# Optimization experiments

Hardware: AMD Instinct MI355X
Metric: run time of the kernel (lower is better)

The kernel has to match this reference:

```python
import jax, jax.numpy as jnp
import numpy as np

B, C, H, W = 4, 3, 1024, 1024


def softsplat_sum(im, flow):
    """Summation forward-warp (softsplat, no metric): bilinear scatter-add.
    im: [B,C,H,W], flow: [B,2,H,W] (flow[:,0]=dx, flow[:,1]=dy)."""
    b, c, h, w = im.shape
    n = h * w
    X = jnp.arange(w, dtype=flow.dtype)[None, None, :] + flow[:, 0]  # [B,H,W]
    Y = jnp.arange(h, dtype=flow.dtype)[None, :, None] + flow[:, 1]  # [B,H,W]
    x0 = jnp.floor(X); y0 = jnp.floor(Y)
    x1 = x0 + 1.0;     y1 = y0 + 1.0
    # bilinear weights for the 4 surrounding integer pixels: NW, NE, SW, SE
    ws = jnp.stack([(x1 - X) * (y1 - Y), (X - x0) * (y1 - Y),
                    (x1 - X) * (Y - y0), (X - x0) * (Y - y0)])  # [4,B,H,W]
    xi = jnp.stack([x0, x1, x0, x1]).astype(jnp.int32)
    yi = jnp.stack([y0, y0, y1, y1]).astype(jnp.int32)
    valid = (xi >= 0) & (xi < w) & (yi >= 0) & (yi < h)
    ws = jnp.where(valid, ws, 0.0)
    idx = jnp.clip(yi, 0, h - 1) * w + jnp.clip(xi, 0, w - 1)     # [4,B,H,W]
    idx = idx.reshape(4, b, n).transpose(1, 0, 2)                  # [B,4,N]
    ws = ws.reshape(4, b, n).transpose(1, 0, 2)                    # [B,4,N]
    imf = im.reshape(b, c, n)

    def splat_one(imf_b, idx_b, w_b):
        vals = (imf_b[:, None, :] * w_b[None]).reshape(c, 4 * n)   # [C,4N]
        return jnp.zeros((c, n), imf_b.dtype).at[:, idx_b.reshape(-1)].add(vals)

    out = jax.vmap(splat_one)(imf, idx, ws)                        # [B,C,N]
    return out.reshape(b, c, h, w)


def setup_inputs() -> dict:
    key = jax.random.key(0)
    k1, k2, k3, k4 = jax.random.split(key, 4)
    flows = 5.0 * jax.random.normal(k1, (2, B, 2, H, W), jnp.float32)
    im0 = jax.random.uniform(k2, (B, C, H, W), jnp.float32)
    im1 = jax.random.uniform(k3, (B, C, H, W), jnp.float32)
    t_value = 0.2 + 0.6 * jax.random.uniform(k4, (B,), jnp.float32)
    return {"flows": flows, "im0": im0, "im1": im1, "t_value": t_value}


def reference(flows, im0, im1, t_value):
    t = t_value.reshape(-1, 1, 1, 1)
    warped_fir = softsplat_sum(im0, (1.0 / t) * flows[0])
    warped_sec = softsplat_sum(im1, (1.0 / (1.0 - t)) * flows[1])
    loss = jnp.mean(jnp.abs(warped_fir - im1)) + jnp.mean(jnp.abs(warped_sec - im0))
    return loss
```

## Files before the change

### kernel.cpp

```cpp
#include <hip/hip_runtime.h>

#define BN 4
#define CN 3
#define HN 1024
#define WN 1024
#define HW (HN * WN)
#define BHW (BN * HW)
#define TOT (BN * CN * HW)

#define TS 64
#define TXN 16
#define TYN 16
#define NTB 256
#define NTILE 1024
#define CHUNK 4096
#define NCHB 1024
#define NPAIR 8

#define OFF_GCNT 0
#define OFF_LOSS 8192
#define OFF_TICK 8200
#define OFF_BORD 8448
#define SZ_BORDR (BN * 16 * 1024 * 8)
#define OFF_REC  (OFF_BORD + 4 * SZ_BORDR)

#define INV_BSCALE (1.0f / 65536.0f)
#define FMASK 0x1FFFFFull

#define PQ 252.0f
#define INV_PQ (1.0f / 252.0f)
#define VQ 4095.0f
#define VSCL (65536.0f / 4095.0f)

__device__ __forceinline__ float blockReduce4(float local, float* smem) {
#pragma unroll
    for (int off = 32; off > 0; off >>= 1)
        local += __shfl_down(local, off, 64);
    int wave = threadIdx.x >> 6;
    if ((threadIdx.x & 63) == 0) smem[wave] = local;
    __syncthreads();
    float s = 0.0f;
    if (threadIdx.x == 0)
        s = smem[0] + smem[1] + smem[2] + smem[3];
    return s;
}

__global__ __launch_bounds__(256) void p1_kernel(
    const float* __restrict__ flows,
    const float* __restrict__ im0,
    const float* __restrict__ im1,
    const float* __restrict__ tv,
    unsigned int* __restrict__ gcnt,
    unsigned long long* __restrict__ rec,
    int cap, int dirsel)
{
    __shared__ unsigned int cnt[NTB];
    __shared__ unsigned int off[NTB];
    __shared__ unsigned int sexc[NTB];
    __shared__ unsigned int stot;
    __shared__ unsigned char sbkt[CHUNK];
    __shared__ unsigned long long stage[CHUNK];
    int tid = threadIdx.x;
    cnt[tid] = 0;
    __syncthreads();

    int bid = blockIdx.x;
    int dir, chunk;
    if (dirsel == 2) { dir = bid >> 10; chunk = bid & 1023; }
    else             { dir = dirsel;    chunk = bid; }

    const float* flow = flows + (size_t)dir * (BN * 2 * HW);
    const float* im   = dir ? im1 : im0;
    unsigned int* gk  = gcnt + dir * NTILE;
    unsigned long long* recd =
        rec + (size_t)((dirsel == 2) ? dir : 0) * NTILE * (size_t)cap;

    int base = chunk * CHUNK;
    int b = base >> 20;
    int pb = base - b * HW;
    float t = tv[b];
    float s = dir ? (1.0f / (1.0f - t)) : (1.0f / t);
    const float2* fxp = (const float2*)(flow + (size_t)(b * 2 + 0) * HW);
    const float2* fyp = (const float2*)(flow + (size_t)(b * 2 + 1) * HW);
    const float2* v0p = (const float2*)(im + (size_t)(b * 3 + 0) * HW);
    const float2* v1p = (const float2*)(im + (size_t)(b * 3 + 1) * HW);
    const float2* v2p = (const float2*)(im + (size_t)(b * 3 + 2) * HW);

    unsigned sc[2 * NPAIR];
    unsigned long long pay[2 * NPAIR];

#pragma unroll
    for (int i = 0; i < NPAIR; ++i) {
        int p0 = pb + 2 * tid + i * 512;
        int y = p0 >> 10;
        int x = p0 & 1023;
        int e = p0 >> 1;
        float2 fx2 = fxp[e], fy2 = fyp[e];
        float2 c02 = v0p[e], c12 = v1p[e], c22 = v2p[e];
        float Xh[2], Yh[2], vv0[2], vv1[2], vv2[2];
        Xh[0] = (float)x + s * fx2.x;        Xh[1] = (float)(x + 1) + s * fx2.y;
        Yh[0] = (float)y + s * fy2.x;        Yh[1] = (float)y + s * fy2.y;
        vv0[0] = c02.x; vv0[1] = c02.y;
        vv1[0] = c12.x; vv1[1] = c12.y;
        vv2[0] = c22.x; vv2[1] = c22.y;
        int kk[2]; bool val[2];
#pragma unroll
        for (int h = 0; h < 2; ++h) {
            int x0 = (int)floorf(Xh[h]);
            int y0 = (int)floorf(Yh[h]);
            val[h] = !(x0 < -1 || x0 > WN - 1 || y0 < -1 || y0 > HN - 1);
            int bx = (x0 < 0 ? 0 : x0) >> 6;
            int by = (y0 < 0 ? 0 : y0) >> 6;
            kk[h] = (by << 4) + bx;
            float lx = Xh[h] - (float)(bx << 6);
            float ly = Yh[h] - (float)(by << 6);
            unsigned long long lq = __float2uint_rn((lx + 1.0f) * PQ);
            unsigned long long mq = __float2uint_rn((ly + 1.0f) * PQ);
            unsigned long long q0 = __float2uint_rn(vv0[h] * VQ);
            unsigned long long q1 = __float2uint_rn(vv1[h] * VQ);
            unsigned long long q2 = __float2uint_rn(vv2[h] * VQ);
            pay[2 * i + h] = lq | (mq << 14) | (q0 << 28) | (q1 << 40) | (q2 << 52);
        }
        if (val[0] & val[1] & (kk[0] == kk[1])) {
            unsigned ls = atomicAdd(&cnt[kk[0]], 2u);
            sc[2 * i]     = ((unsigned)kk[0] << 16) | ls;
            sc[2 * i + 1] = ((unsigned)kk[0] << 16) | (ls + 1u);
        } else {
            sc[2 * i]     = val[0] ? (((unsigned)kk[0] << 16) | atomicAdd(&cnt[kk[0]], 1u))
                                   : 0xFFFFFFFFu;
            sc[2 * i + 1] = val[1] ? (((unsigned)kk[1] << 16) | atomicAdd(&cnt[kk[1]], 1u))
                                   : 0xFFFFFFFFu;
        }
    }
    __syncthreads();

    unsigned c = cnt[tid];
    unsigned g = c ? atomicAdd(&gk[b * NTB + tid], c) : 0u;
    if (tid < 64) {
        unsigned v0 = cnt[4 * tid], v1 = cnt[4 * tid + 1];
        unsigned v2 = cnt[4 * tid + 2], v3 = cnt[4 * tid + 3];
        unsigned s01 = v0 + v1;
        unsigned tot = s01 + v2 + v3;
        unsigned run = tot;
#pragma unroll
        for (int d = 1; d < 64; d <<= 1) {
            unsigned u = __shfl_up(run, d, 64);
            if (tid >= d) run += u;
        }
        unsigned excl = run - tot;
        sexc[4 * tid]     = excl;
        sexc[4 * tid + 1] = excl + v0;
        sexc[4 * tid + 2] = excl + s01;
        sexc[4 * tid + 3] = excl + s01 + v2;
        if (tid == 63) stot = run;
    }
    off[tid] = g;
    __syncthreads();

#pragma unroll
    for (int j = 0; j < 2 * NPAIR; ++j) {
        unsigned scv = sc[j];
        if (scv == 0xFFFFFFFFu) continue;
        unsigned k = scv >> 16;
        unsigned pos = sexc[k] + (scv & 0xFFFFu);
        stage[pos] = pay[j];
        sbkt[pos] = (unsigned char)k;
    }
    __syncthreads();

    unsigned T = stot;
    for (unsigned j = tid; j < T; j += 256) {
        int k2 = sbkt[j];
        unsigned slot = off[k2] + (j - sexc[k2]);
        if (slot < (unsigned)cap)
            recd[(size_t)(b * NTB + k2) * (size_t)cap + slot] = stage[j];
    }
}

__global__ __launch_bounds__(256) void p2_kernel(
    const unsigned long long* __restrict__ rec,
    const unsigned int* __restrict__ gcnt,
    const float* __restrict__ im0,
    const float* __restrict__ im1,
    unsigned long long* __restrict__ bord,
    double* __restrict__ loss,
    int cap, int dirsel)
{
    __shared__ unsigned long long tileu[65 * 65];
    __shared__ float smem4[4];
    int kb = blockIdx.x;
    int dir, k;
    if (dirsel == 2) { dir = kb >> 10; k = kb & 1023; }
    else             { dir = dirsel;   k = kb; }
    const float* ref = dir ? im0 : im1;
    const unsigned long long* recd =
        rec + (size_t)((dirsel == 2) ? dir : 0) * NTILE * (size_t)cap;
    unsigned long long* rowacc = bord + (size_t)(2 * dir)     * (BN * 16 * 1024);
    unsigned long long* colacc = bord + (size_t)(2 * dir + 1) * (BN * 16 * 1024);

    int b  = k >> 8;
    int by = (k >> 4) & 15;
    int bx = k & 15;
    int tx = bx << 6, ty = by << 6;
    int tid = threadIdx.x;

    for (int i = tid; i < 65 * 65; i += 256) tileu[i] = 0ull;
    __syncthreads();

    unsigned n = gcnt[dir * NTILE + k];
    if (n > (unsigned)cap) n = cap;
    const unsigned long long* rk = recd + (size_t)k * (size_t)cap;
    for (unsigned r = tid; r < n; r += 256) {
        unsigned long long w = rk[r];
        float lx = (float)(unsigned)(w & 0x3FFFu)         * INV_PQ - 1.0f;
        float ly = (float)(unsigned)((w >> 14) & 0x3FFFu) * INV_PQ - 1.0f;
        float v0s = (float)(unsigned)((w >> 28) & 0xFFFu) * VSCL;
        float v1s = (float)(unsigned)((w >> 40) & 0xFFFu) * VSCL;
        float v2s = (float)(unsigned)((w >> 52) & 0xFFFu) * VSCL;
        int i0 = (int)floorf(lx); if (i0 > 63) i0 = 63;
        int j0 = (int)floorf(ly); if (j0 > 63) j0 = 63;
        float fx = lx - (float)i0;
        float fy = ly - (float)j0;
        float wx0 = 1.0f - fx, wy0 = 1.0f - fy;
#pragma unroll
        for (int c = 0; c < 4; ++c) {
            int ii = i0 + (c & 1), jj = j0 + (c >> 1);
            float w4 = (c & 1 ? fx : wx0) * (c >> 1 ? fy : wy0);
            if (ii >= 0 && jj >= 0 && tx + ii < WN && ty + jj < HN) {
                unsigned long long pk =
                      (unsigned long long)__float2uint_rn(v0s * w4)
                    | ((unsigned long long)__float2uint_rn(v1s * w4) << 21)
                    | ((unsigned long long)__float2uint_rn(v2s * w4) << 42);
                atomicAdd(&tileu[jj * 65 + ii], pk);
            }
        }
    }
    __syncthreads();

    float local = 0.0f;
    for (int c = tid; c < 65 * 65; c += 256) {
        int j = c / 65, i = c - j * 65;
        int gx = tx + i, gy = ty + j;
        if (gx >= WN || gy >= HN) continue;
        unsigned long long a = tileu[c];
        bool fin_i = (i >= 1 || bx == 0) && (i <= 63);
        bool fin_j = (j >= 1 || by == 0) && (j <= 63);
        if (fin_i && fin_j) {
            float a0 = (float)(unsigned)(a & FMASK)         * INV_BSCALE;
            float a1 = (float)(unsigned)((a >> 21) & FMASK) * INV_BSCALE;
            float a2 = (float)(unsigned)((a >> 42) & FMASK) * INV_BSCALE;
            size_t o = (size_t)gy * WN + gx;
            local += fabsf(a0 - ref[(size_t)(b * 3 + 0) * HW + o])
                   + fabsf(a1 - ref[(size_t)(b * 3 + 1) * HW + o])
                   + fabsf(a2 - ref[(size_t)(b * 3 + 2) * HW + o]);
        } else if (a) {
            if ((gy & 63) == 0 && gy >= 64)
                atomicAdd(&rowacc[((size_t)(b * 16 + (gy >> 6)) << 10) + gx], a);
            else
                atomicAdd(&colacc[((size_t)(b * 16 + (gx >> 6)) << 10) + gy], a);
        }
    }
    float ssum = blockReduce4(local, smem4);
    if (tid == 0) unsafeAtomicAdd(loss, (double)ssum);
}

__global__ __launch_bounds__(256) void border_kernel(
    const unsigned long long* __restrict__ bord,
    const float* __restrict__ ref0,
    const float* __restrict__ ref1,
    double* __restrict__ loss,
    unsigned int* __restrict__ ticket,
    float* __restrict__ out)
{
    __shared__ float smem4[4];
    int idx = blockIdx.x * 256 + threadIdx.x;
    int reg = idx >> 16;
    int e = idx & 0xFFFF;
    bool isrow = (reg & 1) == 0;
    const float* ref = (reg < 2) ? ref0 : ref1;
    unsigned long long a = bord[idx];
    int b = e >> 14;
    int rc = (e >> 10) & 15;
    int q = e & 1023;
    float local = 0.0f;
    bool process;
    int gx, gy;
    if (isrow) { process = (rc >= 1); gy = rc << 6; gx = q; }
    else       { process = (rc >= 1) && !(((q & 63) == 0) && q >= 64); gx = rc << 6; gy = q; }
    if (process && a) {
        float a0 = (float)(unsigned)(a & FMASK)         * INV_BSCALE;
        float a1 = (float)(unsigned)((a >> 21) & FMASK) * INV_BSCALE;
        float a2 = (float)(unsigned)((a >> 42) & FMASK) * INV_BSCALE;
        size_t o = (size_t)gy * WN + gx;
        local += fabsf(a0 - ref[(size_t)(b * 3 + 0) * HW + o])
               + fabsf(a1 - ref[(size_t)(b * 3 + 1) * HW + o])
               + fabsf(a2 - ref[(size_t)(b * 3 + 2) * HW + o]);
    } else if (process) {
        size_t o = (size_t)gy * WN + gx;
        local += fabsf(ref[(size_t)(b * 3 + 0) * HW + o])
               + fabsf(ref[(size_t)(b * 3 + 1) * HW + o])
               + fabsf(ref[(size_t)(b * 3 + 2) * HW + o]);
    }
    float ssum = blockReduce4(local, smem4);
    if (threadIdx.x == 0) {
        unsafeAtomicAdd(loss, (double)ssum);
        __threadfence();
        unsigned tkt = atomicAdd(ticket, 1u);
        if (tkt == gridDim.x - 1) {
            double v = unsafeAtomicAdd(loss, 0.0);
            out[0] = (float)(v / (double)TOT);
        }
    }
}

#define FPSCALE 65536.0f
#define INV_FPSCALE (1.0f / 65536.0f)

__device__ __forceinline__ unsigned long long pack3f(float c0, float c1, float c2, float w) {
    unsigned long long f0 = (unsigned long long)__float2uint_rn(c0 * w * FPSCALE);
    unsigned long long f1 = (unsigned long long)__float2uint_rn(c1 * w * FPSCALE);
    unsigned long long f2 = (unsigned long long)__float2uint_rn(c2 * w * FPSCALE);
    return f0 | (f1 << 21) | (f2 << 42);
}

__global__ __launch_bounds__(256) void splat_kernel(
    const float* __restrict__ flow, const float* __restrict__ im,
    const float* __restrict__ tv, unsigned long long* __restrict__ acc, int invert)
{
    int gid = blockIdx.x * blockDim.x + threadIdx.x;
    if (gid >= BHW) return;
    int b = gid / HW;
    int p = gid - b * HW;
    int y = p >> 10, x = p & 1023;
    float t = tv[b];
    float s = invert ? (1.0f / (1.0f - t)) : (1.0f / t);
    float X = (float)x + s * flow[(size_t)(b * 2 + 0) * HW + p];
    float Y = (float)y + s * flow[(size_t)(b * 2 + 1) * HW + p];
    float x0f = floorf(X), y0f = floorf(Y);
    int x0 = (int)x0f, y0 = (int)y0f;
    float fx = X - x0f, fy = Y - y0f;
    float wx0 = 1.0f - fx, wx1 = fx, wy0 = 1.0f - fy, wy1 = fy;
    float v0 = im[(size_t)(b * 3 + 0) * HW + p];
    float v1 = im[(size_t)(b * 3 + 1) * HW + p];
    float v2 = im[(size_t)(b * 3 + 2) * HW + p];
    bool vx0 = (x0 >= 0) & (x0 < WN);
    bool vx1 = (x0 + 1 >= 0) & (x0 + 1 < WN);
    unsigned long long* accb = acc + (size_t)b * HW;
#pragma unroll
    for (int r = 0; r < 2; ++r) {
        int yi = y0 + r;
        if (yi < 0 || yi >= HN) continue;
        float wy = r ? wy1 : wy0;
        size_t rowbase = (size_t)yi * WN;
        if (vx0) atomicAdd(&accb[rowbase + x0],     pack3f(v0, v1, v2, wx0 * wy));
        if (vx1) atomicAdd(&accb[rowbase + x0 + 1], pack3f(v0, v1, v2, wx1 * wy));
    }
}

__global__ __launch_bounds__(256) void loss_kernel(
    unsigned long long* __restrict__ acc, const float* __restrict__ ref,
    double* __restrict__ loss)
{
    __shared__ float smem4[4];
    int stride = gridDim.x * blockDim.x;
    float local = 0.0f;
    for (int i = blockIdx.x * blockDim.x + threadIdx.x; i < BHW; i += stride) {
        int b = i / HW;
        int p = i - b * HW;
        unsigned long long a = acc[i];
        acc[i] = 0ull;
        float c0 = (float)(unsigned)(a & FMASK)         * INV_FPSCALE;
        float c1 = (float)(unsigned)((a >> 21) & FMASK) * INV_FPSCALE;
        float c2 = (float)(unsigned)((a >> 42) & FMASK) * INV_FPSCALE;
        local += fabsf(c0 - ref[(size_t)(b * 3 + 0) * HW + p])
               + fabsf(c1 - ref[(size_t)(b * 3 + 1) * HW + p])
               + fabsf(c2 - ref[(size_t)(b * 3 + 2) * HW + p]);
    }
    float ssum = blockReduce4(local, smem4);
    if (threadIdx.x == 0) unsafeAtomicAdd(loss, (double)ssum);
}

__global__ void finalize_kernel(const double* __restrict__ loss,
                                float* __restrict__ out)
{
    out[0] = (float)(loss[0] / (double)TOT);
}

extern "C" void kernel_launch(void* const* d_in, const int* in_sizes, int n_in,
                              void* d_out, int out_size, void* d_ws, size_t ws_size,
                              hipStream_t stream)
{
    const float* flows = (const float*)d_in[0];
    const float* im0   = (const float*)d_in[1];
    const float* im1   = (const float*)d_in[2];
    const float* tv    = (const float*)d_in[3];
    const float* flows1 = flows + (size_t)BN * 2 * HW;
    const int threads = 256;

    long long avail = (long long)ws_size - (long long)OFF_REC;
    int capBoth = 0, capSeq = 0;
    if (avail > 0) {
        long long cb = avail / (2LL * NTILE * 8);
        long long cs = avail / ((long long)NTILE * 8);
        capBoth = (int)(cb > 8192 ? 8192 : cb);
        capSeq  = (int)(cs > 8192 ? 8192 : cs);
    }

    char* ws = (char*)d_ws;
    unsigned int* gcnt = (unsigned int*)(ws + OFF_GCNT);
    double* loss = (double*)(ws + OFF_LOSS);
    unsigned int* ticket = (unsigned int*)(ws + OFF_TICK);
    unsigned long long* bord = (unsigned long long*)(ws + OFF_BORD);
    unsigned long long* rec = (unsigned long long*)(ws + OFF_REC);

    if (capBoth >= 5120) {
        hipMemsetAsync(d_ws, 0, OFF_REC, stream);
        p1_kernel<<<2 * NCHB, threads, 0, stream>>>(flows, im0, im1, tv,
                                                    gcnt, rec, capBoth, 2);
        p2_kernel<<<2 * NTILE, threads, 0, stream>>>(rec, gcnt, im0, im1,
                                                     bord, loss, capBoth, 2);
        border_kernel<<<1024, threads, 0, stream>>>(bord, im1, im0, loss,
                                                    ticket, (float*)d_out);
    } else if (capSeq >= 5120) {
        hipMemsetAsync(d_ws, 0, OFF_REC, stream);
        p1_kernel<<<NCHB, threads, 0, stream>>>(flows, im0, im1, tv,
                                                gcnt, rec, capSeq, 0);
        p2_kernel<<<NTILE, threads, 0, stream>>>(rec, gcnt, im0, im1,
                                                 bord, loss, capSeq, 0);
        p1_kernel<<<NCHB, threads, 0, stream>>>(flows, im0, im1, tv,
                                                gcnt, rec, capSeq, 1);
        p2_kernel<<<NTILE, threads, 0, stream>>>(rec, gcnt, im0, im1,
                                                 bord, loss, capSeq, 1);
        border_kernel<<<1024, threads, 0, stream>>>(bord, im1, im0, loss,
                                                    ticket, (float*)d_out);
    } else {
        unsigned long long* acc = (unsigned long long*)d_ws;
        double* lss = (double*)(acc + (size_t)BN * HW);
        hipMemsetAsync(d_ws, 0, sizeof(unsigned long long) * (size_t)BN * HW + sizeof(double), stream);
        const int sgrid = (BHW + threads - 1) / threads;
        splat_kernel<<<sgrid, threads, 0, stream>>>(flows, im0, tv, acc, 0);
        loss_kernel<<<2048, threads, 0, stream>>>(acc, im1, lss);
        splat_kernel<<<sgrid, threads, 0, stream>>>(flows1, im1, tv, acc, 1);
        loss_kernel<<<2048, threads, 0, stream>>>(acc, im0, lss);
        finalize_kernel<<<1, 1, 0, stream>>>(lss, (float*)d_out);
    }
}
```

Measured before the change: 296.9 us.

## Fuse bin, tile-splat and border passes into one persistent kernel with grid barriers

```diff
diff --git a/kernel.cpp b/kernel.cpp
--- a/kernel.cpp
+++ b/kernel.cpp
@@ -16,10 +16,13 @@
 #define CHUNK 4096
 #define NCHB 1024
 #define NPAIR 8
+#define NBLK 1024
 
 #define OFF_GCNT 0
 #define OFF_LOSS 8192
 #define OFF_TICK 8200
+#define OFF_BAR1 8204
+#define OFF_BAR2 8208
 #define OFF_BORD 8448
 #define SZ_BORDR (BN * 16 * 1024 * 8)
 #define OFF_REC  (OFF_BORD + 4 * SZ_BORDR)
@@ -32,6 +35,22 @@
 #define VQ 4095.0f
 #define VSCL (65536.0f / 4095.0f)
 
+struct P1Sh {
+    unsigned int cnt[NTB];
+    unsigned int off[NTB];
+    unsigned int sexc[NTB];
+    unsigned int stot;
+    unsigned char sbkt[CHUNK];
+    unsigned long long stage[CHUNK];
+};
+struct Sh {
+    union {
+        P1Sh p1;
+        unsigned long long tileu[65 * 65];
+    } u;
+    float smem4[4];
+};
+
 __device__ __forceinline__ float blockReduce4(float local, float* smem) {
 #pragma unroll
     for (int off = 32; off > 0; off >>= 1)
@@ -45,35 +64,35 @@
     return s;
 }
 
-__global__ __launch_bounds__(256) void p1_kernel(
-    const float* __restrict__ flows,
-    const float* __restrict__ im0,
-    const float* __restrict__ im1,
-    const float* __restrict__ tv,
-    unsigned int* __restrict__ gcnt,
-    unsigned long long* __restrict__ rec,
-    int cap, int dirsel)
-{
-    __shared__ unsigned int cnt[NTB];
-    __shared__ unsigned int off[NTB];
-    __shared__ unsigned int sexc[NTB];
-    __shared__ unsigned int stot;
-    __shared__ unsigned char sbkt[CHUNK];
-    __shared__ unsigned long long stage[CHUNK];
+__device__ __forceinline__ void gbar(unsigned int* ctr, unsigned int target) {
+    __syncthreads();
+    if (threadIdx.x == 0) {
+        __threadfence();
+        atomicAdd(ctr, 1u);
+        while (__hip_atomic_load(ctr, __ATOMIC_RELAXED,
+                                 __HIP_MEMORY_SCOPE_AGENT) < target)
+            __builtin_amdgcn_s_sleep(2);
+        __threadfence();
+    }
+    __syncthreads();
+}
+
+__device__ __forceinline__ void p1_work(
+    Sh& sh, int chunk,
+    const float* __restrict__ flow,
+    const float* __restrict__ im,
+    const float* __restrict__ tv, int dir,
+    unsigned int* __restrict__ gk,
+    unsigned long long* __restrict__ recd, int cap)
+{
     int tid = threadIdx.x;
+    unsigned int* cnt = sh.u.p1.cnt;
+    unsigned int* off = sh.u.p1.off;
+    unsigned int* sexc = sh.u.p1.sexc;
+    unsigned char* sbkt = sh.u.p1.sbkt;
+    unsigned long long* stage = sh.u.p1.stage;
     cnt[tid] = 0;
     __syncthreads();
-
-    int bid = blockIdx.x;
-    int dir, chunk;
-    if (dirsel == 2) { dir = bid >> 10; chunk = bid & 1023; }
-    else             { dir = dirsel;    chunk = bid; }
-
-    const float* flow = flows + (size_t)dir * (BN * 2 * HW);
-    const float* im   = dir ? im1 : im0;
-    unsigned int* gk  = gcnt + dir * NTILE;
-    unsigned long long* recd =
-        rec + (size_t)((dirsel == 2) ? dir : 0) * NTILE * (size_t)cap;
 
     int base = chunk * CHUNK;
     int b = base >> 20;
@@ -152,7 +171,7 @@
         sexc[4 * tid + 1] = excl + v0;
         sexc[4 * tid + 2] = excl + s01;
         sexc[4 * tid + 3] = excl + s01 + v2;
-        if (tid == 63) stot = run;
+        if (tid == 63) sh.u.p1.stot = run;
     }
     off[tid] = g;
     __syncthreads();
@@ -168,36 +187,26 @@
     }
     __syncthreads();
 
-    unsigned T = stot;
+    unsigned T = sh.u.p1.stot;
     for (unsigned j = tid; j < T; j += 256) {
         int k2 = sbkt[j];
         unsigned slot = off[k2] + (j - sexc[k2]);
         if (slot < (unsigned)cap)
             recd[(size_t)(b * NTB + k2) * (size_t)cap + slot] = stage[j];
     }
-}
-
-__global__ __launch_bounds__(256) void p2_kernel(
-    const unsigned long long* __restrict__ rec,
-    const unsigned int* __restrict__ gcnt,
-    const float* __restrict__ im0,
-    const float* __restrict__ im1,
-    unsigned long long* __restrict__ bord,
-    double* __restrict__ loss,
-    int cap, int dirsel)
-{
-    __shared__ unsigned long long tileu[65 * 65];
-    __shared__ float smem4[4];
-    int kb = blockIdx.x;
-    int dir, k;
-    if (dirsel == 2) { dir = kb >> 10; k = kb & 1023; }
-    else             { dir = dirsel;   k = kb; }
-    const float* ref = dir ? im0 : im1;
-    const unsigned long long* recd =
-        rec + (size_t)((dirsel == 2) ? dir : 0) * NTILE * (size_t)cap;
-    unsigned long long* rowacc = bord + (size_t)(2 * dir)     * (BN * 16 * 1024);
-    unsigned long long* colacc = bord + (size_t)(2 * dir + 1) * (BN * 16 * 1024);
-
+    __syncthreads();
+}
+
+__device__ __forceinline__ void p2_work(
+    Sh& sh, int k,
+    const unsigned long long* __restrict__ recd,
+    const unsigned int* __restrict__ gk,
+    const float* __restrict__ ref,
+    unsigned long long* __restrict__ rowacc,
+    unsigned long long* __restrict__ colacc,
+    double* __restrict__ loss, int cap)
+{
+    unsigned long long* tileu = sh.u.tileu;
     int b  = k >> 8;
     int by = (k >> 4) & 15;
     int bx = k & 15;
@@ -207,7 +216,7 @@
     for (int i = tid; i < 65 * 65; i += 256) tileu[i] = 0ull;
     __syncthreads();
 
-    unsigned n = gcnt[dir * NTILE + k];
+    unsigned n = gk[k];
     if (n > (unsigned)cap) n = cap;
     const unsigned long long* rk = recd + (size_t)k * (size_t)cap;
     for (unsigned r = tid; r < n; r += 256) {
@@ -260,11 +269,13 @@
                 atomicAdd(&colacc[((size_t)(b * 16 + (gx >> 6)) << 10) + gy], a);
         }
     }
-    float ssum = blockReduce4(local, smem4);
+    float ssum = blockReduce4(local, sh.smem4);
     if (tid == 0) unsafeAtomicAdd(loss, (double)ssum);
-}
-
-__global__ __launch_bounds__(256) void border_kernel(
+    __syncthreads();
+}
+
+__device__ __forceinline__ void border_work(
+    Sh& sh, int bid,
     const unsigned long long* __restrict__ bord,
     const float* __restrict__ ref0,
     const float* __restrict__ ref1,
@@ -272,8 +283,7 @@
     unsigned int* __restrict__ ticket,
     float* __restrict__ out)
 {
-    __shared__ float smem4[4];
-    int idx = blockIdx.x * 256 + threadIdx.x;
+    int idx = bid * 256 + threadIdx.x;
     int reg = idx >> 16;
     int e = idx & 0xFFFF;
     bool isrow = (reg & 1) == 0;
@@ -301,16 +311,94 @@
                + fabsf(ref[(size_t)(b * 3 + 1) * HW + o])
                + fabsf(ref[(size_t)(b * 3 + 2) * HW + o]);
     }
-    float ssum = blockReduce4(local, smem4);
+    float ssum = blockReduce4(local, sh.smem4);
     if (threadIdx.x == 0) {
         unsafeAtomicAdd(loss, (double)ssum);
         __threadfence();
         unsigned tkt = atomicAdd(ticket, 1u);
-        if (tkt == gridDim.x - 1) {
+        if (tkt == NBLK - 1) {
             double v = unsafeAtomicAdd(loss, 0.0);
             out[0] = (float)(v / (double)TOT);
         }
     }
+}
+
+__global__ __launch_bounds__(256, 4) void mega_kernel(
+    const float* __restrict__ flows,
+    const float* __restrict__ im0,
+    const float* __restrict__ im1,
+    const float* __restrict__ tv,
+    char* __restrict__ ws,
+    float* __restrict__ out,
+    int cap)
+{
+    __shared__ Sh sh;
+    int bid = blockIdx.x;
+
+    unsigned int* gcnt = (unsigned int*)(ws + OFF_GCNT);
+    double* loss = (double*)(ws + OFF_LOSS);
+    unsigned int* ticket = (unsigned int*)(ws + OFF_TICK);
+    unsigned int* bar1 = (unsigned int*)(ws + OFF_BAR1);
+    unsigned int* bar2 = (unsigned int*)(ws + OFF_BAR2);
+    unsigned long long* bord = (unsigned long long*)(ws + OFF_BORD);
+    unsigned long long* rec = (unsigned long long*)(ws + OFF_REC);
+
+#pragma unroll 1
+    for (int d = 0; d < 2; ++d) {
+        const float* flow = flows + (size_t)d * (BN * 2 * HW);
+        const float* im   = d ? im1 : im0;
+        p1_work(sh, bid, flow, im, tv, d, gcnt + d * NTILE,
+                rec + (size_t)d * NTILE * (size_t)cap, cap);
+    }
+    gbar(bar1, NBLK);
+
+#pragma unroll 1
+    for (int d = 0; d < 2; ++d) {
+        const float* ref = d ? im0 : im1;
+        unsigned long long* rowacc = bord + (size_t)(2 * d)     * (BN * 16 * 1024);
+        unsigned long long* colacc = bord + (size_t)(2 * d + 1) * (BN * 16 * 1024);
+        p2_work(sh, bid, rec + (size_t)d * NTILE * (size_t)cap,
+                gcnt + d * NTILE, ref, rowacc, colacc, loss, cap);
+    }
+    gbar(bar2, NBLK);
+
+    border_work(sh, bid, bord, im1, im0, loss, ticket, out);
+}
+
+__global__ __launch_bounds__(256) void p1_kernel(
+    const float* __restrict__ flows, const float* __restrict__ im0,
+    const float* __restrict__ im1, const float* __restrict__ tv,
+    unsigned int* __restrict__ gcnt, unsigned long long* __restrict__ rec,
+    int cap, int dir)
+{
+    __shared__ Sh sh;
+    const float* flow = flows + (size_t)dir * (BN * 2 * HW);
+    const float* im   = dir ? im1 : im0;
+    p1_work(sh, blockIdx.x, flow, im, tv, dir, gcnt + dir * NTILE, rec, cap);
+}
+
+__global__ __launch_bounds__(256) void p2_kernel(
+    const unsigned long long* __restrict__ rec,
+    const unsigned int* __restrict__ gcnt,
+    const float* __restrict__ im0, const float* __restrict__ im1,
+    unsigned long long* __restrict__ bord, double* __restrict__ loss,
+    int cap, int dir)
+{
+    __shared__ Sh sh;
+    const float* ref = dir ? im0 : im1;
+    unsigned long long* rowacc = bord + (size_t)(2 * dir)     * (BN * 16 * 1024);
+    unsigned long long* colacc = bord + (size_t)(2 * dir + 1) * (BN * 16 * 1024);
+    p2_work(sh, blockIdx.x, rec, gcnt + dir * NTILE, ref, rowacc, colacc, loss, cap);
+}
+
+__global__ __launch_bounds__(256) void border_kernel(
+    const unsigned long long* __restrict__ bord,
+    const float* __restrict__ ref0, const float* __restrict__ ref1,
+    double* __restrict__ loss, unsigned int* __restrict__ ticket,
+    float* __restrict__ out)
+{
+    __shared__ Sh sh;
+    border_work(sh, blockIdx.x, bord, ref0, ref1, loss, ticket, out);
 }
 
 #define FPSCALE 65536.0f
@@ -415,12 +503,8 @@
 
     if (capBoth >= 5120) {
         hipMemsetAsync(d_ws, 0, OFF_REC, stream);
-        p1_kernel<<<2 * NCHB, threads, 0, stream>>>(flows, im0, im1, tv,
-                                                    gcnt, rec, capBoth, 2);
-        p2_kernel<<<2 * NTILE, threads, 0, stream>>>(rec, gcnt, im0, im1,
-                                                     bord, loss, capBoth, 2);
-        border_kernel<<<1024, threads, 0, stream>>>(bord, im1, im0, loss,
-                                                    ticket, (float*)d_out);
+        mega_kernel<<<NBLK, threads, 0, stream>>>(flows, im0, im1, tv,
+                                                  ws, (float*)d_out, capBoth);
     } else if (capSeq >= 5120) {
         hipMemsetAsync(d_ws, 0, OFF_REC, stream);
         p1_kernel<<<NCHB, threads, 0, stream>>>(flows, im0, im1, tv,
```

Result: slower. 727.9 us (+145.1%).
